# Kernel tuning notes

Measured on AMD Instinct MI355X. Metric: run time of the kernel, lower is better.

The kernel has to match this reference:

```python
import jax, jax.numpy as jnp
import numpy as np

DIM = 128      # transformer_dim = bottleneck_ch
NHEADS = 4
NEXP = 16
EHID = 256
WS = 8         # window_size
EPS = 1e-5     # LayerNorm eps


def setup_inputs() -> dict:
    key = jax.random.key(0)
    ks = jax.random.split(key, 6)
    B, H, W = 2, 128, 128
    N = H * W
    s = 0.02
    return {
        "x": jax.random.normal(ks[0], (B, N, DIM), jnp.float32),
        "ln1_g": jnp.ones((DIM,), jnp.float32),
        "ln1_b": jnp.zeros((DIM,), jnp.float32),
        "w_qkv": jax.random.normal(ks[1], (3 * DIM, DIM), jnp.float32) * s,
        "b_qkv": jnp.zeros((3 * DIM,), jnp.float32),
        "w_proj": jax.random.normal(ks[2], (DIM, DIM), jnp.float32) * s,
        "b_proj": jnp.zeros((DIM,), jnp.float32),
        "ln2_g": jnp.ones((DIM,), jnp.float32),
        "ln2_b": jnp.zeros((DIM,), jnp.float32),
        "gate_w": jax.random.normal(ks[3], (NEXP, DIM), jnp.float32) * s,
        "w1": jax.random.normal(ks[4], (NEXP, EHID, DIM), jnp.float32) * s,
        "b1": jnp.zeros((NEXP, EHID), jnp.float32),
        "w2": jax.random.normal(ks[5], (NEXP, DIM, EHID), jnp.float32) * s,
        "b2": jnp.zeros((NEXP, DIM), jnp.float32),
        "H": H,
        "W": W,
    }


def _ln(x, g, b):
    m = jnp.mean(x, axis=-1, keepdims=True)
    v = jnp.var(x, axis=-1, keepdims=True)
    return (x - m) * jax.lax.rsqrt(v + EPS) * g + b


def _win_attn(x, H, W, w_qkv, b_qkv, w_proj, b_proj):
    # x: (B, N, C); H,W divisible by WS (no padding branch needed)
    B, N, C = x.shape
    hd = C // NHEADS
    nH, nW = H // WS, W // WS
    # window partition: (B, N, C) -> (B*nH*nW, WS*WS, C)
    xw = x.reshape(B, nH, WS, nW, WS, C).transpose(0, 1, 3, 2, 4, 5)
    xw = xw.reshape(B * nH * nW, WS * WS, C)
    qkv = xw @ w_qkv.T + b_qkv
    q, k, v = jnp.split(qkv, 3, axis=-1)
    def heads(t):
        return t.reshape(-1, WS * WS, NHEADS, hd).transpose(0, 2, 1, 3)
    q, k, v = heads(q), heads(k), heads(v)
    scores = jnp.einsum('whqd,whkd->whqk', q, k) / jnp.sqrt(jnp.float32(hd))
    a = jax.nn.softmax(scores, axis=-1)
    o = jnp.einsum('whqk,whkd->whqd', a, v).transpose(0, 2, 1, 3)
    o = o.reshape(-1, WS * WS, C) @ w_proj.T + b_proj
    # window merge back to (B, N, C)
    o = o.reshape(B, nH, nW, WS, WS, C).transpose(0, 1, 3, 2, 4, 5)
    return o.reshape(B, N, C)


def _moe(x, gate_w, w1, b1, w2, b2):
    # top_k = 1 routing, eval mode (no noise / aux losses)
    B, N, C = x.shape
    f = x.reshape(-1, C)                      # (T, C)
    logits = f @ gate_w.T                     # (T, E)
    probs = jax.nn.softmax(logits, axis=-1)
    p = jnp.max(probs, axis=-1)               # top-1 prob
    idx = jnp.argmax(probs, axis=-1)          # top-1 expert id
    wgt = p / (p + 1e-8)                      # top_k_probs / (sum + eps)
    out = jnp.zeros_like(f)
    for e in range(NEXP):                     # small fixed expert loop
        h = jax.nn.gelu(f @ w1[e].T + b1[e], approximate=False)
        eo = h @ w2[e].T + b2[e]
        out = out + jnp.where((idx == e)[:, None], eo, 0.0)
    return (out * wgt[:, None]).reshape(B, N, C)


def reference(x, ln1_g, ln1_b, w_qkv, b_qkv, w_proj, b_proj,
              ln2_g, ln2_b, gate_w, w1, b1, w2, b2, H, W):
    x = x + _win_attn(_ln(x, ln1_g, ln1_b), H, W, w_qkv, b_qkv, w_proj, b_proj)
    x = x + _moe(_ln(x, ln2_g, ln2_b), gate_w, w1, b1, w2, b2)
    return x
```

## Files before the change

kernel.cpp:

```cpp
#include <hip/hip_runtime.h>
#include <math.h>

#define T_TOK 32768
#define DIM 128
#define NHEADS 4
#define HD 32
#define NEXP 16
#define EHID 256
#define NWIN 512
#define EPS 1e-5f
#define CPAD 16

typedef _Float16 f16x8 __attribute__((ext_vector_type(8)));
typedef _Float16 f16x4 __attribute__((ext_vector_type(4)));
typedef float f32x4v __attribute__((ext_vector_type(4)));

#define MFMA16(a, b, c) __builtin_amdgcn_mfma_f32_16x16x32_f16(a, b, c, 0, 0, 0)
#define LO_SCALE 4096.0f
#define LO_INV (1.0f / 4096.0f)

__device__ __forceinline__ int sw128(int r, int c) {
    return r * 128 + (((c >> 3) ^ (r & 7)) << 3) + (c & 7);
}
__device__ __forceinline__ int sw64(int r, int c) {
    return r * 64 + (((c >> 3) ^ (r & 7)) << 3) + (c & 7);
}
__device__ __forceinline__ int swht(int tok, int hid) {
    return tok * 256 + (((hid >> 3) ^ (tok & 7)) << 3) + (hid & 7);
}

__global__ __launch_bounds__(256) void k_cvt(
    const float* __restrict__ wqkv, const float* __restrict__ wproj,
    const float* __restrict__ w1, const float* __restrict__ w2,
    _Float16* __restrict__ wq_h, _Float16* __restrict__ wq_l,
    _Float16* __restrict__ wp_h, _Float16* __restrict__ wp_l,
    _Float16* __restrict__ w1h, _Float16* __restrict__ w2h,
    int* __restrict__ counts)
{
    int i = blockIdx.x * 256 + threadIdx.x;
    if (blockIdx.x == 0 && threadIdx.x < NEXP * CPAD) counts[threadIdx.x] = 0;
    {
        float4 a = ((const float4*)w1)[i];
        f16x4 h;
        h[0] = (_Float16)a.x; h[1] = (_Float16)a.y; h[2] = (_Float16)a.z; h[3] = (_Float16)a.w;
        *(f16x4*)(w1h + (size_t)i * 4) = h;
        float4 b = ((const float4*)w2)[i];
        f16x4 h2;
        h2[0] = (_Float16)b.x; h2[1] = (_Float16)b.y; h2[2] = (_Float16)b.z; h2[3] = (_Float16)b.w;
        *(f16x4*)(w2h + (size_t)i * 4) = h2;
    }
    if (i < 3 * DIM * DIM / 4) {
        float4 f = ((const float4*)wqkv)[i];
        float fv[4] = {f.x, f.y, f.z, f.w};
        f16x4 h, l;
        #pragma unroll
        for (int j = 0; j < 4; ++j) {
            _Float16 hh = (_Float16)fv[j];
            h[j] = hh;
            l[j] = (_Float16)((fv[j] - (float)hh) * LO_SCALE);
        }
        *(f16x4*)(wq_h + (size_t)i * 4) = h;
        *(f16x4*)(wq_l + (size_t)i * 4) = l;
    }
    if (i < DIM * DIM / 4) {
        float4 f = ((const float4*)wproj)[i];
        float fv[4] = {f.x, f.y, f.z, f.w};
        f16x4 h, l;
        #pragma unroll
        for (int j = 0; j < 4; ++j) {
            _Float16 hh = (_Float16)fv[j];
            h[j] = hh;
            l[j] = (_Float16)((fv[j] - (float)hh) * LO_SCALE);
        }
        *(f16x4*)(wp_h + (size_t)i * 4) = h;
        *(f16x4*)(wp_l + (size_t)i * 4) = l;
    }
}

__global__ __launch_bounds__(512) void k_attn(
    const float* __restrict__ x,
    const float* __restrict__ ln_g, const float* __restrict__ ln_b,
    const _Float16* __restrict__ wq_h, const _Float16* __restrict__ wq_l,
    const float* __restrict__ b_qkv,
    const _Float16* __restrict__ wp_h, const _Float16* __restrict__ wp_l,
    const float* __restrict__ b_proj,
    const float* __restrict__ ln2_g, const float* __restrict__ ln2_b,
    const float* __restrict__ gw,
    float* __restrict__ x2, _Float16* __restrict__ y2,
    float* __restrict__ wgt, int* __restrict__ perm, int* __restrict__ counts)
{
    __shared__ __align__(16) char smem[131072];
    _Float16* xoh = (_Float16*)(smem);
    _Float16* xol = (_Float16*)(smem + 16384);
    _Float16* qh  = (_Float16*)(smem + 32768);
    _Float16* ql  = (_Float16*)(smem + 49152);
    _Float16* kh  = (_Float16*)(smem + 65536);
    _Float16* kl  = (_Float16*)(smem + 81920);
    _Float16* vth = (_Float16*)(smem + 98304);
    _Float16* vtl = (_Float16*)(smem + 114688);
    float* xf   = (float*)(smem + 32768);
    float* ylds = (float*)(smem + 65792);
    float* lgs  = (float*)(smem + 98816);

    int tid = threadIdx.x;
    int w = tid >> 6, lane = tid & 63;
    int l15 = lane & 15, lg = lane >> 4;
    int wid = blockIdx.x;
    int wb = wid >> 8, wrr = (wid >> 4) & 15, wcc = wid & 15;
    const int tokbase = wb * 16384 + wrr * 1024 + wcc * 8;
    const size_t base = (size_t)tokbase * DIM;

    f16x8 qbh[3][4], qbl[3][4];
    float qbias[3];
    #pragma unroll
    for (int ct = 0; ct < 3; ++ct) {
        int o = w * 48 + ct * 16 + l15;
        qbias[ct] = b_qkv[o];
        #pragma unroll
        for (int ks = 0; ks < 4; ++ks) {
            size_t wo = (size_t)o * DIM + ks * 32 + lg * 8;
            qbh[ct][ks] = *(const f16x8*)(wq_h + wo);
            qbl[ct][ks] = *(const f16x8*)(wq_l + wo);
        }
    }
    float xres[16];
    {
        int rt = w & 3, cb = (w >> 2) * 64;
        #pragma unroll
        for (int ct = 0; ct < 4; ++ct) {
            int c = cb + ct * 16 + l15;
            #pragma unroll
            for (int r = 0; r < 4; ++r) {
                int q = rt * 16 + lg * 4 + r;
                xres[ct * 4 + r] = x[base + (size_t)(q >> 3) * 16384 + (size_t)(q & 7) * DIM + c];
            }
        }
    }

    {
        int tt = tid >> 3, sub = tid & 7;
        const float* xr = x + base + (size_t)(tt >> 3) * 16384 + (size_t)(tt & 7) * DIM + sub * 16;
        float v[16];
        float s = 0.f, sq = 0.f;
        #pragma unroll
        for (int j = 0; j < 4; ++j) {
            float4 t4 = *(const float4*)(xr + j * 4);
            v[4 * j] = t4.x; v[4 * j + 1] = t4.y; v[4 * j + 2] = t4.z; v[4 * j + 3] = t4.w;
            s += (t4.x + t4.y) + (t4.z + t4.w);
            sq = fmaf(t4.x, t4.x, fmaf(t4.y, t4.y, fmaf(t4.z, t4.z, fmaf(t4.w, t4.w, sq))));
        }
        s += __shfl_xor(s, 1); sq += __shfl_xor(sq, 1);
        s += __shfl_xor(s, 2); sq += __shfl_xor(sq, 2);
        s += __shfl_xor(s, 4); sq += __shfl_xor(sq, 4);
        float m = s * (1.f / DIM);
        float var = sq * (1.f / DIM) - m * m;
        float rs = rsqrtf(var + EPS);
        _Float16 hh[16], ll[16];
        #pragma unroll
        for (int j = 0; j < 16; ++j) {
            int k = sub * 16 + j;
            float a = (v[j] - m) * rs * ln_g[k] + ln_b[k];
            _Float16 h = (_Float16)a;
            hh[j] = h;
            ll[j] = (_Float16)((a - (float)h) * LO_SCALE);
        }
        *(f16x8*)&xoh[sw128(tt, sub * 16)]     = *(const f16x8*)&hh[0];
        *(f16x8*)&xoh[sw128(tt, sub * 16 + 8)] = *(const f16x8*)&hh[8];
        *(f16x8*)&xol[sw128(tt, sub * 16)]     = *(const f16x8*)&ll[0];
        *(f16x8*)&xol[sw128(tt, sub * 16 + 8)] = *(const f16x8*)&ll[8];
    }
    __syncthreads();

    #pragma unroll
    for (int ct = 0; ct < 3; ++ct) {
        int o = w * 48 + ct * 16 + l15;
        f32x4v am[4], ac[4];
        #pragma unroll
        for (int rt = 0; rt < 4; ++rt) { am[rt] = 0.0f; ac[rt] = 0.0f; }
        #pragma unroll
        for (int rt = 0; rt < 4; ++rt) {
            #pragma unroll
            for (int ks = 0; ks < 4; ++ks) {
                f16x8 ah = *(const f16x8*)&xoh[sw128(rt * 16 + l15, ks * 32 + lg * 8)];
                f16x8 al = *(const f16x8*)&xol[sw128(rt * 16 + l15, ks * 32 + lg * 8)];
                am[rt] = MFMA16(ah, qbh[ct][ks], am[rt]);
                ac[rt] = MFMA16(ah, qbl[ct][ks], ac[rt]);
                ac[rt] = MFMA16(al, qbh[ct][ks], ac[rt]);
            }
        }
        float bias = qbias[ct];
        if (o < 256) {
            #pragma unroll
            for (int rt = 0; rt < 4; ++rt) {
                #pragma unroll
                for (int r = 0; r < 4; ++r) {
                    int row = rt * 16 + lg * 4 + r;
                    float val = am[rt][r] + ac[rt][r] * LO_INV + bias;
                    _Float16 h = (_Float16)val;
                    _Float16 lo = (_Float16)((val - (float)h) * LO_SCALE);
                    if (o < 128) { qh[sw128(row, o)] = h;       ql[sw128(row, o)] = lo; }
                    else         { kh[sw128(row, o - 128)] = h; kl[sw128(row, o - 128)] = lo; }
                }
            }
        } else {
            int d = o - 256;
            #pragma unroll
            for (int rt = 0; rt < 4; ++rt) {
                f16x4 vh4, vl4;
                #pragma unroll
                for (int r = 0; r < 4; ++r) {
                    float val = am[rt][r] + ac[rt][r] * LO_INV + bias;
                    _Float16 h = (_Float16)val;
                    vh4[r] = h;
                    vl4[r] = (_Float16)((val - (float)h) * LO_SCALE);
                }
                int tok0 = rt * 16 + lg * 4;
                *(f16x4*)&vth[sw64(d, tok0)] = vh4;
                *(f16x4*)&vtl[sw64(d, tok0)] = vl4;
            }
        }
    }
    __syncthreads();

    const float scale = 0.17677669529663687f;
    int h = w & 3;
    int qo = h * HD, rgb = (w >> 2) * 2;
    float preg[2][4][4];
    {
        f16x8 kbh[4], kbl[4];
        #pragma unroll
        for (int ct = 0; ct < 4; ++ct) {
            kbh[ct] = *(const f16x8*)&kh[sw128(ct * 16 + l15, qo + lg * 8)];
            kbl[ct] = *(const f16x8*)&kl[sw128(ct * 16 + l15, qo + lg * 8)];
        }
        #pragma unroll
        for (int t = 0; t < 2; ++t) {
            int rg = rgb + t;
            f16x8 qah = *(const f16x8*)&qh[sw128(rg * 16 + l15, qo + lg * 8)];
            f16x8 qal = *(const f16x8*)&ql[sw128(rg * 16 + l15, qo + lg * 8)];
            f32x4v sm[4], sc2[4];
            #pragma unroll
            for (int ct = 0; ct < 4; ++ct) {
                sm[ct] = 0.0f; sc2[ct] = 0.0f;
                sm[ct] = MFMA16(qah, kbh[ct], sm[ct]);
                sc2[ct] = MFMA16(qah, kbl[ct], sc2[ct]);
                sc2[ct] = MFMA16(qal, kbh[ct], sc2[ct]);
            }
            #pragma unroll
            for (int r = 0; r < 4; ++r) {
                float v0 = (sm[0][r] + sc2[0][r] * LO_INV) * scale;
                float v1 = (sm[1][r] + sc2[1][r] * LO_INV) * scale;
                float v2 = (sm[2][r] + sc2[2][r] * LO_INV) * scale;
                float v3 = (sm[3][r] + sc2[3][r] * LO_INV) * scale;
                float mx = fmaxf(fmaxf(v0, v1), fmaxf(v2, v3));
                mx = fmaxf(mx, __shfl_xor(mx, 1));
                mx = fmaxf(mx, __shfl_xor(mx, 2));
                mx = fmaxf(mx, __shfl_xor(mx, 4));
                mx = fmaxf(mx, __shfl_xor(mx, 8));
                float e0 = expf(v0 - mx), e1 = expf(v1 - mx), e2 = expf(v2 - mx), e3 = expf(v3 - mx);
                float ss = (e0 + e1) + (e2 + e3);
                ss += __shfl_xor(ss, 1); ss += __shfl_xor(ss, 2);
                ss += __shfl_xor(ss, 4); ss += __shfl_xor(ss, 8);
                float inv = 1.f / ss;
                preg[t][0][r] = e0 * inv;
                preg[t][1][r] = e1 * inv;
                preg[t][2][r] = e2 * inv;
                preg[t][3][r] = e3 * inv;
            }
        }
    }
    __syncthreads();

    {
        _Float16* dsth = (h < 2) ? qh : kh;
        _Float16* dstl = (h < 2) ? ql : kl;
        int pb = (h & 1) * 4096;
        #pragma unroll
        for (int t = 0; t < 2; ++t) {
            int rg = rgb + t;
            #pragma unroll
            for (int ct = 0; ct < 4; ++ct) {
                #pragma unroll
                for (int r = 0; r < 4; ++r) {
                    float p = preg[t][ct][r];
                    int row = rg * 16 + lg * 4 + r, col = ct * 16 + l15;
                    _Float16 hh = (_Float16)p;
                    dsth[pb + sw64(row, col)] = hh;
                    dstl[pb + sw64(row, col)] = (_Float16)((p - (float)hh) * LO_SCALE);
                }
            }
        }
    }

    {
        const _Float16* psh = (h < 2) ? qh : kh;
        const _Float16* psl = (h < 2) ? ql : kl;
        int pb = (h & 1) * 4096;
        f16x8 vbh[2][2], vbl[2][2];
        #pragma unroll
        for (int ks = 0; ks < 2; ++ks)
            #pragma unroll
            for (int ct = 0; ct < 2; ++ct) {
                vbh[ks][ct] = *(const f16x8*)&vth[sw64(qo + ct * 16 + l15, ks * 32 + lg * 8)];
                vbl[ks][ct] = *(const f16x8*)&vtl[sw64(qo + ct * 16 + l15, ks * 32 + lg * 8)];
            }
        #pragma unroll
        for (int t = 0; t < 2; ++t) {
            int rg = rgb + t;
            f32x4v om[2], oc[2];
            om[0] = 0.0f; om[1] = 0.0f; oc[0] = 0.0f; oc[1] = 0.0f;
            #pragma unroll
            for (int ks = 0; ks < 2; ++ks) {
                f16x8 pah = *(const f16x8*)&psh[pb + sw64(rg * 16 + l15, ks * 32 + lg * 8)];
                f16x8 pal = *(const f16x8*)&psl[pb + sw64(rg * 16 + l15, ks * 32 + lg * 8)];
                #pragma unroll
                for (int ct = 0; ct < 2; ++ct) {
                    om[ct] = MFMA16(pah, vbh[ks][ct], om[ct]);
                    oc[ct] = MFMA16(pah, vbl[ks][ct], oc[ct]);
                    oc[ct] = MFMA16(pal, vbh[ks][ct], oc[ct]);
                }
            }
            #pragma unroll
            for (int ct = 0; ct < 2; ++ct) {
                #pragma unroll
                for (int r = 0; r < 4; ++r) {
                    float val = om[ct][r] + oc[ct][r] * LO_INV;
                    int row = rg * 16 + lg * 4 + r, col = qo + ct * 16 + l15;
                    _Float16 hh = (_Float16)val;
                    xoh[sw128(row, col)] = hh;
                    xol[sw128(row, col)] = (_Float16)((val - (float)hh) * LO_SCALE);
                }
            }
        }
    }

    f16x8 wpbh[4][4], wpbl[4][4];
    float pbias[4];
    {
        int cb = (w >> 2) * 64;
        #pragma unroll
        for (int ct = 0; ct < 4; ++ct) {
            int c = cb + ct * 16 + l15;
            pbias[ct] = b_proj[c];
            #pragma unroll
            for (int ks = 0; ks < 4; ++ks) {
                wpbh[ct][ks] = *(const f16x8*)(wp_h + (size_t)c * DIM + ks * 32 + lg * 8);
                wpbl[ct][ks] = *(const f16x8*)(wp_l + (size_t)c * DIM + ks * 32 + lg * 8);
            }
        }
    }
    __syncthreads();

    {
        int rt = w & 3, cb = (w >> 2) * 64;
        f32x4v pm[4], pc[4];
        #pragma unroll
        for (int ct = 0; ct < 4; ++ct) { pm[ct] = 0.0f; pc[ct] = 0.0f; }
        #pragma unroll
        for (int ks = 0; ks < 4; ++ks) {
            f16x8 ah = *(const f16x8*)&xoh[sw128(rt * 16 + l15, ks * 32 + lg * 8)];
            f16x8 al = *(const f16x8*)&xol[sw128(rt * 16 + l15, ks * 32 + lg * 8)];
            #pragma unroll
            for (int ct = 0; ct < 4; ++ct) {
                pm[ct] = MFMA16(ah, wpbh[ct][ks], pm[ct]);
                pc[ct] = MFMA16(ah, wpbl[ct][ks], pc[ct]);
                pc[ct] = MFMA16(al, wpbh[ct][ks], pc[ct]);
            }
        }
        #pragma unroll
        for (int ct = 0; ct < 4; ++ct) {
            int c = cb + ct * 16 + l15;
            #pragma unroll
            for (int r = 0; r < 4; ++r) {
                int q = rt * 16 + lg * 4 + r;
                xf[q * 129 + c] = xres[ct * 4 + r] + (pm[ct][r] + pc[ct][r] * LO_INV + pbias[ct]);
            }
        }
    }
    __syncthreads();

    float vrow[16];
    _Float16 yh[16];
    {
        int tt = tid >> 3, sub = tid & 7;
        const float* xr = xf + tt * 129 + sub * 16;
        float s = 0.f, sq = 0.f;
        #pragma unroll
        for (int j = 0; j < 16; ++j) {
            float t = xr[j];
            vrow[j] = t;
            s += t;
            sq = fmaf(t, t, sq);
        }
        s += __shfl_xor(s, 1); sq += __shfl_xor(sq, 1);
        s += __shfl_xor(s, 2); sq += __shfl_xor(sq, 2);
        s += __shfl_xor(s, 4); sq += __shfl_xor(sq, 4);
        float m = s * (1.f / DIM);
        float var = sq * (1.f / DIM) - m * m;
        float rs = rsqrtf(var + EPS);
        #pragma unroll
        for (int j = 0; j < 16; ++j) {
            int k = sub * 16 + j;
            float a = (vrow[j] - m) * rs * ln2_g[k] + ln2_b[k];
            ylds[tt * 129 + k] = a;
            yh[j] = (_Float16)a;
        }
    }
    __syncthreads();

    {
        int tk = tid & 63, eg = tid >> 6;
        const float* g0 = gw + (eg * 2 + 0) * DIM;
        const float* g1 = gw + (eg * 2 + 1) * DIM;
        float a0 = 0.f, a1 = 0.f;
        #pragma unroll 8
        for (int k = 0; k < DIM; ++k) {
            float yv = ylds[tk * 129 + k];
            a0 = fmaf(yv, g0[k], a0);
            a1 = fmaf(yv, g1[k], a1);
        }
        lgs[tk * 20 + eg * 2]     = a0;
        lgs[tk * 20 + eg * 2 + 1] = a1;
    }
    __syncthreads();

    if (tid < 64) {
        float mx = -1e30f; int am = 0;
        #pragma unroll
        for (int e = 0; e < NEXP; ++e) {
            float v = lgs[tid * 20 + e];
            if (v > mx) { mx = v; am = e; }
        }
        float ss = 0.f;
        #pragma unroll
        for (int e = 0; e < NEXP; ++e) ss += expf(lgs[tid * 20 + e] - mx);
        float p = 1.f / ss;
        int gtok = tokbase + (tid >> 3) * 128 + (tid & 7);
        wgt[gtok] = p / (p + 1e-8f);

        int myrank = 0, mycnt = 0;
        #pragma unroll
        for (int e = 0; e < NEXP; ++e) {
            unsigned long long mask = __ballot(am == e);
            if (am == e) myrank = (int)__popcll(mask & ((1ull << tid) - 1));
            if (tid == e) mycnt = (int)__popcll(mask);
        }
        int bky = 0;
        if (tid < NEXP) bky = atomicAdd(&counts[tid * CPAD], mycnt);
        bky = __shfl(bky, am);
        perm[(size_t)am * T_TOK + bky + myrank] = gtok;
    }

    {
        int tt = tid >> 3, sub = tid & 7;
        int gtok = tokbase + (tt >> 3) * 128 + (tt & 7);
        float4* dst = (float4*)(x2 + (size_t)gtok * DIM + sub * 16);
        #pragma unroll
        for (int j = 0; j < 4; ++j)
            dst[j] = make_float4(vrow[4 * j], vrow[4 * j + 1], vrow[4 * j + 2], vrow[4 * j + 3]);
        *(f16x8*)(y2 + (size_t)gtok * DIM + sub * 16)     = *(const f16x8*)&yh[0];
        *(f16x8*)(y2 + (size_t)gtok * DIM + sub * 16 + 8) = *(const f16x8*)&yh[8];
    }
}

__global__ __launch_bounds__(256, 3) void k_expert(
    const _Float16* __restrict__ y2, const float* __restrict__ x2,
    const _Float16* __restrict__ w1h, const float* __restrict__ b1,
    const _Float16* __restrict__ w2h, const float* __restrict__ b2,
    const int* __restrict__ perm, const int* __restrict__ counts,
    const float* __restrict__ wgt, float* __restrict__ out)
{
    __shared__ _Float16 yt[64 * 128];
    __shared__ _Float16 ht[64 * 256];
    __shared__ int rows[64];

    int bflat = blockIdx.x;
    int e = -1, tile = 0, acc0 = 0;
    #pragma unroll
    for (int ee = 0; ee < NEXP; ++ee) {
        int t = (counts[ee * CPAD] + 63) >> 6;
        if (e < 0 && bflat < acc0 + t) { e = ee; tile = bflat - acc0; }
        acc0 += t;
    }
    if (e < 0) return;
    int cnt = counts[e * CPAD];
    int row0 = tile << 6;
    int nr = min(64, cnt - row0);
    int tid = threadIdx.x, wv = tid >> 6, lane = tid & 63;
    int l15 = lane & 15, lg = lane >> 4;

    if (tid < 64) rows[tid] = (tid < nr) ? perm[(size_t)e * T_TOK + row0 + tid] : 0;
    __syncthreads();
    f16x8 vz = (_Float16)0.0f;
    for (int i = tid; i < 1024; i += 256) {
        int tt = i >> 4, k = (i & 15) * 8;
        f16x8 val = vz;
        if (tt < nr) val = *(const f16x8*)(y2 + (size_t)rows[tt] * DIM + k);
        *(f16x8*)&yt[sw128(tt, k)] = val;
    }
    __syncthreads();

    {
        f16x8 yb[4][4];
        #pragma unroll
        for (int ct = 0; ct < 4; ++ct)
            #pragma unroll
            for (int ks = 0; ks < 4; ++ks)
                yb[ct][ks] = *(const f16x8*)&yt[sw128(ct * 16 + l15, ks * 32 + lg * 8)];
        #pragma unroll
        for (int rt = 0; rt < 4; ++rt) {
            int hid_row = wv * 64 + rt * 16 + l15;
            f16x8 a1[4];
            #pragma unroll
            for (int ks = 0; ks < 4; ++ks)
                a1[ks] = *(const f16x8*)(w1h + ((size_t)e * EHID + hid_row) * DIM + ks * 32 + lg * 8);
            f32x4v acc[4];
            #pragma unroll
            for (int ct = 0; ct < 4; ++ct) acc[ct] = 0.0f;
            #pragma unroll
            for (int ct = 0; ct < 4; ++ct)
                #pragma unroll
                for (int ks = 0; ks < 4; ++ks)
                    acc[ct] = MFMA16(a1[ks], yb[ct][ks], acc[ct]);
            int hid0 = wv * 64 + rt * 16 + lg * 4;
            float4 bb4 = *(const float4*)(b1 + e * EHID + hid0);
            float bbv[4] = {bb4.x, bb4.y, bb4.z, bb4.w};
            #pragma unroll
            for (int ct = 0; ct < 4; ++ct) {
                f16x4 hv;
                #pragma unroll
                for (int r = 0; r < 4; ++r) {
                    float a = acc[ct][r] + bbv[r];
                    float gl = 0.5f * a * (1.f + erff(a * 0.70710678118654752f));
                    hv[r] = (_Float16)gl;
                }
                int tok = ct * 16 + l15;
                *(f16x4*)&ht[swht(tok, hid0)] = hv;
            }
        }
    }
    __syncthreads();

    {
        f16x8 wb[2][8];
        #pragma unroll
        for (int ct = 0; ct < 2; ++ct) {
            int c = wv * 32 + ct * 16 + l15;
            #pragma unroll
            for (int ks = 0; ks < 8; ++ks)
                wb[ct][ks] = *(const f16x8*)(w2h + ((size_t)e * DIM + c) * EHID + ks * 32 + lg * 8);
        }
        #pragma unroll
        for (int rt = 0; rt < 4; ++rt) {
            f16x8 af[8];
            #pragma unroll
            for (int ks = 0; ks < 8; ++ks)
                af[ks] = *(const f16x8*)&ht[swht(rt * 16 + l15, ks * 32 + lg * 8)];
            f32x4v acc2[2];
            acc2[0] = 0.0f; acc2[1] = 0.0f;
            #pragma unroll
            for (int ks = 0; ks < 8; ++ks)
                #pragma unroll
                for (int ct = 0; ct < 2; ++ct)
                    acc2[ct] = MFMA16(af[ks], wb[ct][ks], acc2[ct]);
            #pragma unroll
            for (int ct = 0; ct < 2; ++ct) {
                int c = wv * 32 + ct * 16 + l15;
                float bb = b2[e * DIM + c];
                #pragma unroll
                for (int r = 0; r < 4; ++r) {
                    int tt = rt * 16 + lg * 4 + r;
                    if (tt < nr) {
                        int gtok = rows[tt];
                        size_t go = (size_t)gtok * DIM + c;
                        out[go] = x2[go] + wgt[gtok] * (acc2[ct][r] + bb);
                    }
                }
            }
        }
    }
}

extern "C" void kernel_launch(void* const* d_in, const int* in_sizes, int n_in,
                              void* d_out, int out_size, void* d_ws, size_t ws_size,
                              hipStream_t stream) {
    const float* x      = (const float*)d_in[0];
    const float* ln1_g  = (const float*)d_in[1];
    const float* ln1_b  = (const float*)d_in[2];
    const float* w_qkv  = (const float*)d_in[3];
    const float* b_qkv  = (const float*)d_in[4];
    const float* w_proj = (const float*)d_in[5];
    const float* b_proj = (const float*)d_in[6];
    const float* ln2_g  = (const float*)d_in[7];
    const float* ln2_b  = (const float*)d_in[8];
    const float* gate_w = (const float*)d_in[9];
    const float* w1     = (const float*)d_in[10];
    const float* b1     = (const float*)d_in[11];
    const float* w2     = (const float*)d_in[12];
    const float* b2     = (const float*)d_in[13];
    float* out = (float*)d_out;

    char* p = (char*)d_ws;
    float* x2 = (float*)p;                 p += (size_t)T_TOK * DIM * 4;
    _Float16* y2 = (_Float16*)p;           p += (size_t)T_TOK * DIM * 2;
    _Float16* wq_h = (_Float16*)p;         p += 3 * DIM * DIM * 2;
    _Float16* wq_l = (_Float16*)p;         p += 3 * DIM * DIM * 2;
    _Float16* wp_h = (_Float16*)p;         p += DIM * DIM * 2;
    _Float16* wp_l = (_Float16*)p;         p += DIM * DIM * 2;
    _Float16* w1h = (_Float16*)p;          p += NEXP * EHID * DIM * 2;
    _Float16* w2h = (_Float16*)p;          p += NEXP * EHID * DIM * 2;
    float* wgt = (float*)p;                p += T_TOK * 4;
    int* perm = (int*)p;                   p += (size_t)NEXP * T_TOK * 4;
    int* counts = (int*)p;                 p += NEXP * CPAD * 4;

    k_cvt<<<512, 256, 0, stream>>>(w_qkv, w_proj, w1, w2, wq_h, wq_l, wp_h, wp_l,
                                   w1h, w2h, counts);
    k_attn<<<NWIN, 512, 0, stream>>>(x, ln1_g, ln1_b, wq_h, wq_l, b_qkv,
                                     wp_h, wp_l, b_proj, ln2_g, ln2_b, gate_w,
                                     x2, y2, wgt, perm, counts);
    k_expert<<<544, 256, 0, stream>>>(y2, x2, w1h, b1, w2h, b2, perm, counts, wgt, out);
}
```

Baseline: 114.1 us.

## Double attention block to 1024 threads, splitting per-wave work in half

The window-attention kernel now runs 16 waves per block instead of 8. QKV projection, score/softmax, PV, output projection, LayerNorm and gate-logit work are each split across the extra waves, so every wave handles half as many tiles. The goal is more latency hiding and fewer registers per thread for a grid of only 512 blocks, at the cost of more barrier participants and an uneven QKV split (waves 8-15 do one tile, waves 0-7 do two).

```diff
diff --git a/kernel.cpp b/kernel.cpp
--- a/kernel.cpp
+++ b/kernel.cpp
@@ -77,7 +77,7 @@
     }
 }
 
-__global__ __launch_bounds__(512) void k_attn(
+__global__ __launch_bounds__(1024) void k_attn(
     const float* __restrict__ x,
     const float* __restrict__ ln_g, const float* __restrict__ ln_b,
     const _Float16* __restrict__ wq_h, const _Float16* __restrict__ wq_l,
@@ -110,24 +110,25 @@
     const int tokbase = wb * 16384 + wrr * 1024 + wcc * 8;
     const size_t base = (size_t)tokbase * DIM;
 
-    f16x8 qbh[3][4], qbl[3][4];
-    float qbias[3];
+    f16x8 qbh[2][4], qbl[2][4];
+    float qbias[2];
     #pragma unroll
-    for (int ct = 0; ct < 3; ++ct) {
-        int o = w * 48 + ct * 16 + l15;
-        qbias[ct] = b_qkv[o];
+    for (int tl = 0; tl < 2; ++tl) {
+        if (tl == 1 && w >= 8) break;
+        int o = ((tl == 0) ? w : 16 + w) * 16 + l15;
+        qbias[tl] = b_qkv[o];
         #pragma unroll
         for (int ks = 0; ks < 4; ++ks) {
             size_t wo = (size_t)o * DIM + ks * 32 + lg * 8;
-            qbh[ct][ks] = *(const f16x8*)(wq_h + wo);
-            qbl[ct][ks] = *(const f16x8*)(wq_l + wo);
-        }
-    }
-    float xres[16];
-    {
-        int rt = w & 3, cb = (w >> 2) * 64;
-        #pragma unroll
-        for (int ct = 0; ct < 4; ++ct) {
+            qbh[tl][ks] = *(const f16x8*)(wq_h + wo);
+            qbl[tl][ks] = *(const f16x8*)(wq_l + wo);
+        }
+    }
+    float xres[8];
+    {
+        int rt = w & 3, cb = (w >> 2) * 32;
+        #pragma unroll
+        for (int ct = 0; ct < 2; ++ct) {
             int c = cb + ct * 16 + l15;
             #pragma unroll
             for (int r = 0; r < 4; ++r) {
@@ -138,12 +139,12 @@
     }
 
     {
-        int tt = tid >> 3, sub = tid & 7;
-        const float* xr = x + base + (size_t)(tt >> 3) * 16384 + (size_t)(tt & 7) * DIM + sub * 16;
-        float v[16];
+        int tt = tid >> 4, sub = tid & 15;
+        const float* xr = x + base + (size_t)(tt >> 3) * 16384 + (size_t)(tt & 7) * DIM + sub * 8;
+        float v[8];
         float s = 0.f, sq = 0.f;
         #pragma unroll
-        for (int j = 0; j < 4; ++j) {
+        for (int j = 0; j < 2; ++j) {
             float4 t4 = *(const float4*)(xr + j * 4);
             v[4 * j] = t4.x; v[4 * j + 1] = t4.y; v[4 * j + 2] = t4.z; v[4 * j + 3] = t4.w;
             s += (t4.x + t4.y) + (t4.z + t4.w);
@@ -152,28 +153,28 @@
         s += __shfl_xor(s, 1); sq += __shfl_xor(sq, 1);
         s += __shfl_xor(s, 2); sq += __shfl_xor(sq, 2);
         s += __shfl_xor(s, 4); sq += __shfl_xor(sq, 4);
+        s += __shfl_xor(s, 8); sq += __shfl_xor(sq, 8);
         float m = s * (1.f / DIM);
         float var = sq * (1.f / DIM) - m * m;
         float rs = rsqrtf(var + EPS);
-        _Float16 hh[16], ll[16];
-        #pragma unroll
-        for (int j = 0; j < 16; ++j) {
-            int k = sub * 16 + j;
+        _Float16 hh[8], ll[8];
+        #pragma unroll
+        for (int j = 0; j < 8; ++j) {
+            int k = sub * 8 + j;
             float a = (v[j] - m) * rs * ln_g[k] + ln_b[k];
             _Float16 h = (_Float16)a;
             hh[j] = h;
             ll[j] = (_Float16)((a - (float)h) * LO_SCALE);
         }
-        *(f16x8*)&xoh[sw128(tt, sub * 16)]     = *(const f16x8*)&hh[0];
-        *(f16x8*)&xoh[sw128(tt, sub * 16 + 8)] = *(const f16x8*)&hh[8];
-        *(f16x8*)&xol[sw128(tt, sub * 16)]     = *(const f16x8*)&ll[0];
-        *(f16x8*)&xol[sw128(tt, sub * 16 + 8)] = *(const f16x8*)&ll[8];
+        *(f16x8*)&xoh[sw128(tt, sub * 8)] = *(const f16x8*)&hh[0];
+        *(f16x8*)&xol[sw128(tt, sub * 8)] = *(const f16x8*)&ll[0];
     }
     __syncthreads();
 
     #pragma unroll
-    for (int ct = 0; ct < 3; ++ct) {
-        int o = w * 48 + ct * 16 + l15;
+    for (int tl = 0; tl < 2; ++tl) {
+        if (tl == 1 && w >= 8) break;
+        int o = ((tl == 0) ? w : 16 + w) * 16 + l15;
         f32x4v am[4], ac[4];
         #pragma unroll
         for (int rt = 0; rt < 4; ++rt) { am[rt] = 0.0f; ac[rt] = 0.0f; }
@@ -183,12 +184,12 @@
             for (int ks = 0; ks < 4; ++ks) {
                 f16x8 ah = *(const f16x8*)&xoh[sw128(rt * 16 + l15, ks * 32 + lg * 8)];
                 f16x8 al = *(const f16x8*)&xol[sw128(rt * 16 + l15, ks * 32 + lg * 8)];
-                am[rt] = MFMA16(ah, qbh[ct][ks], am[rt]);
-                ac[rt] = MFMA16(ah, qbl[ct][ks], ac[rt]);
-                ac[rt] = MFMA16(al, qbh[ct][ks], ac[rt]);
-            }
-        }
-        float bias = qbias[ct];
+                am[rt] = MFMA16(ah, qbh[tl][ks], am[rt]);
+                ac[rt] = MFMA16(ah, qbl[tl][ks], ac[rt]);
+                ac[rt] = MFMA16(al, qbh[tl][ks], ac[rt]);
+            }
+        }
+        float bias = qbias[tl];
         if (o < 256) {
             #pragma unroll
             for (int rt = 0; rt < 4; ++rt) {
@@ -224,8 +225,8 @@
 
     const float scale = 0.17677669529663687f;
     int h = w & 3;
-    int qo = h * HD, rgb = (w >> 2) * 2;
-    float preg[2][4][4];
+    int qo = h * HD, rg = w >> 2;
+    float preg[4][4];
     {
         f16x8 kbh[4], kbl[4];
         #pragma unroll
@@ -233,40 +234,36 @@
             kbh[ct] = *(const f16x8*)&kh[sw128(ct * 16 + l15, qo + lg * 8)];
             kbl[ct] = *(const f16x8*)&kl[sw128(ct * 16 + l15, qo + lg * 8)];
         }
-        #pragma unroll
-        for (int t = 0; t < 2; ++t) {
-            int rg = rgb + t;
-            f16x8 qah = *(const f16x8*)&qh[sw128(rg * 16 + l15, qo + lg * 8)];
-            f16x8 qal = *(const f16x8*)&ql[sw128(rg * 16 + l15, qo + lg * 8)];
-            f32x4v sm[4], sc2[4];
-            #pragma unroll
-            for (int ct = 0; ct < 4; ++ct) {
-                sm[ct] = 0.0f; sc2[ct] = 0.0f;
-                sm[ct] = MFMA16(qah, kbh[ct], sm[ct]);
-                sc2[ct] = MFMA16(qah, kbl[ct], sc2[ct]);
-                sc2[ct] = MFMA16(qal, kbh[ct], sc2[ct]);
-            }
-            #pragma unroll
-            for (int r = 0; r < 4; ++r) {
-                float v0 = (sm[0][r] + sc2[0][r] * LO_INV) * scale;
-                float v1 = (sm[1][r] + sc2[1][r] * LO_INV) * scale;
-                float v2 = (sm[2][r] + sc2[2][r] * LO_INV) * scale;
-                float v3 = (sm[3][r] + sc2[3][r] * LO_INV) * scale;
-                float mx = fmaxf(fmaxf(v0, v1), fmaxf(v2, v3));
-                mx = fmaxf(mx, __shfl_xor(mx, 1));
-                mx = fmaxf(mx, __shfl_xor(mx, 2));
-                mx = fmaxf(mx, __shfl_xor(mx, 4));
-                mx = fmaxf(mx, __shfl_xor(mx, 8));
-                float e0 = expf(v0 - mx), e1 = expf(v1 - mx), e2 = expf(v2 - mx), e3 = expf(v3 - mx);
-                float ss = (e0 + e1) + (e2 + e3);
-                ss += __shfl_xor(ss, 1); ss += __shfl_xor(ss, 2);
-                ss += __shfl_xor(ss, 4); ss += __shfl_xor(ss, 8);
-                float inv = 1.f / ss;
-                preg[t][0][r] = e0 * inv;
-                preg[t][1][r] = e1 * inv;
-                preg[t][2][r] = e2 * inv;
-                preg[t][3][r] = e3 * inv;
-            }
+        f16x8 qah = *(const f16x8*)&qh[sw128(rg * 16 + l15, qo + lg * 8)];
+        f16x8 qal = *(const f16x8*)&ql[sw128(rg * 16 + l15, qo + lg * 8)];
+        f32x4v sm[4], sc2[4];
+        #pragma unroll
+        for (int ct = 0; ct < 4; ++ct) {
+            sm[ct] = 0.0f; sc2[ct] = 0.0f;
+            sm[ct] = MFMA16(qah, kbh[ct], sm[ct]);
+            sc2[ct] = MFMA16(qah, kbl[ct], sc2[ct]);
+            sc2[ct] = MFMA16(qal, kbh[ct], sc2[ct]);
+        }
+        #pragma unroll
+        for (int r = 0; r < 4; ++r) {
+            float v0 = (sm[0][r] + sc2[0][r] * LO_INV) * scale;
+            float v1 = (sm[1][r] + sc2[1][r] * LO_INV) * scale;
+            float v2 = (sm[2][r] + sc2[2][r] * LO_INV) * scale;
+            float v3 = (sm[3][r] + sc2[3][r] * LO_INV) * scale;
+            float mx = fmaxf(fmaxf(v0, v1), fmaxf(v2, v3));
+            mx = fmaxf(mx, __shfl_xor(mx, 1));
+            mx = fmaxf(mx, __shfl_xor(mx, 2));
+            mx = fmaxf(mx, __shfl_xor(mx, 4));
+            mx = fmaxf(mx, __shfl_xor(mx, 8));
+            float e0 = expf(v0 - mx), e1 = expf(v1 - mx), e2 = expf(v2 - mx), e3 = expf(v3 - mx);
+            float ss = (e0 + e1) + (e2 + e3);
+            ss += __shfl_xor(ss, 1); ss += __shfl_xor(ss, 2);
+            ss += __shfl_xor(ss, 4); ss += __shfl_xor(ss, 8);
+            float inv = 1.f / ss;
+            preg[0][r] = e0 * inv;
+            preg[1][r] = e1 * inv;
+            preg[2][r] = e2 * inv;
+            preg[3][r] = e3 * inv;
         }
     }
     __syncthreads();
@@ -276,18 +273,14 @@
         _Float16* dstl = (h < 2) ? ql : kl;
         int pb = (h & 1) * 4096;
         #pragma unroll
-        for (int t = 0; t < 2; ++t) {
-            int rg = rgb + t;
-            #pragma unroll
-            for (int ct = 0; ct < 4; ++ct) {
-                #pragma unroll
-                for (int r = 0; r < 4; ++r) {
-                    float p = preg[t][ct][r];
-                    int row = rg * 16 + lg * 4 + r, col = ct * 16 + l15;
-                    _Float16 hh = (_Float16)p;
-                    dsth[pb + sw64(row, col)] = hh;
-                    dstl[pb + sw64(row, col)] = (_Float16)((p - (float)hh) * LO_SCALE);
-                }
+        for (int ct = 0; ct < 4; ++ct) {
+            #pragma unroll
+            for (int r = 0; r < 4; ++r) {
+                float p = preg[ct][r];
+                int row = rg * 16 + lg * 4 + r, col = ct * 16 + l15;
+                _Float16 hh = (_Float16)p;
+                dsth[pb + sw64(row, col)] = hh;
+                dstl[pb + sw64(row, col)] = (_Float16)((p - (float)hh) * LO_SCALE);
             }
         }
     }
@@ -304,42 +297,38 @@
                 vbh[ks][ct] = *(const f16x8*)&vth[sw64(qo + ct * 16 + l15, ks * 32 + lg * 8)];
                 vbl[ks][ct] = *(const f16x8*)&vtl[sw64(qo + ct * 16 + l15, ks * 32 + lg * 8)];
             }
-        #pragma unroll
-        for (int t = 0; t < 2; ++t) {
-            int rg = rgb + t;
-            f32x4v om[2], oc[2];
-            om[0] = 0.0f; om[1] = 0.0f; oc[0] = 0.0f; oc[1] = 0.0f;
-            #pragma unroll
-            for (int ks = 0; ks < 2; ++ks) {
-                f16x8 pah = *(const f16x8*)&psh[pb + sw64(rg * 16 + l15, ks * 32 + lg * 8)];
-                f16x8 pal = *(const f16x8*)&psl[pb + sw64(rg * 16 + l15, ks * 32 + lg * 8)];
-                #pragma unroll
-                for (int ct = 0; ct < 2; ++ct) {
-                    om[ct] = MFMA16(pah, vbh[ks][ct], om[ct]);
-                    oc[ct] = MFMA16(pah, vbl[ks][ct], oc[ct]);
-                    oc[ct] = MFMA16(pal, vbh[ks][ct], oc[ct]);
-                }
-            }
+        f32x4v om[2], oc[2];
+        om[0] = 0.0f; om[1] = 0.0f; oc[0] = 0.0f; oc[1] = 0.0f;
+        #pragma unroll
+        for (int ks = 0; ks < 2; ++ks) {
+            f16x8 pah = *(const f16x8*)&psh[pb + sw64(rg * 16 + l15, ks * 32 + lg * 8)];
+            f16x8 pal = *(const f16x8*)&psl[pb + sw64(rg * 16 + l15, ks * 32 + lg * 8)];
             #pragma unroll
             for (int ct = 0; ct < 2; ++ct) {
-                #pragma unroll
-                for (int r = 0; r < 4; ++r) {
-                    float val = om[ct][r] + oc[ct][r] * LO_INV;
-                    int row = rg * 16 + lg * 4 + r, col = qo + ct * 16 + l15;
-                    _Float16 hh = (_Float16)val;
-                    xoh[sw128(row, col)] = hh;
-                    xol[sw128(row, col)] = (_Float16)((val - (float)hh) * LO_SCALE);
-                }
-            }
-        }
-    }
-
-    f16x8 wpbh[4][4], wpbl[4][4];
-    float pbias[4];
-    {
-        int cb = (w >> 2) * 64;
-        #pragma unroll
-        for (int ct = 0; ct < 4; ++ct) {
+                om[ct] = MFMA16(pah, vbh[ks][ct], om[ct]);
+                oc[ct] = MFMA16(pah, vbl[ks][ct], oc[ct]);
+                oc[ct] = MFMA16(pal, vbh[ks][ct], oc[ct]);
+            }
+        }
+        #pragma unroll
+        for (int ct = 0; ct < 2; ++ct) {
+            #pragma unroll
+            for (int r = 0; r < 4; ++r) {
+                float val = om[ct][r] + oc[ct][r] * LO_INV;
+                int row = rg * 16 + lg * 4 + r, col = qo + ct * 16 + l15;
+                _Float16 hh = (_Float16)val;
+                xoh[sw128(row, col)] = hh;
+                xol[sw128(row, col)] = (_Float16)((val - (float)hh) * LO_SCALE);
+            }
+        }
+    }
+
+    f16x8 wpbh[2][4], wpbl[2][4];
+    float pbias[2];
+    {
+        int cb = (w >> 2) * 32;
+        #pragma unroll
+        for (int ct = 0; ct < 2; ++ct) {
             int c = cb + ct * 16 + l15;
             pbias[ct] = b_proj[c];
             #pragma unroll
@@ -352,23 +341,22 @@
     __syncthreads();
 
     {
-        int rt = w & 3, cb = (w >> 2) * 64;
-        f32x4v pm[4], pc[4];
-        #pragma unroll
-        for (int ct = 0; ct < 4; ++ct) { pm[ct] = 0.0f; pc[ct] = 0.0f; }
+        int rt = w & 3, cb = (w >> 2) * 32;
+        f32x4v pm[2], pc[2];
+        pm[0] = 0.0f; pm[1] = 0.0f; pc[0] = 0.0f; pc[1] = 0.0f;
         #pragma unroll
         for (int ks = 0; ks < 4; ++ks) {
             f16x8 ah = *(const f16x8*)&xoh[sw128(rt * 16 + l15, ks * 32 + lg * 8)];
             f16x8 al = *(const f16x8*)&xol[sw128(rt * 16 + l15, ks * 32 + lg * 8)];
             #pragma unroll
-            for (int ct = 0; ct < 4; ++ct) {
+            for (int ct = 0; ct < 2; ++ct) {
                 pm[ct] = MFMA16(ah, wpbh[ct][ks], pm[ct]);
                 pc[ct] = MFMA16(ah, wpbl[ct][ks], pc[ct]);
                 pc[ct] = MFMA16(al, wpbh[ct][ks], pc[ct]);
             }
         }
         #pragma unroll
-        for (int ct = 0; ct < 4; ++ct) {
+        for (int ct = 0; ct < 2; ++ct) {
             int c = cb + ct * 16 + l15;
             #pragma unroll
             for (int r = 0; r < 4; ++r) {
@@ -379,14 +367,14 @@
     }
     __syncthreads();
 
-    float vrow[16];
-    _Float16 yh[16];
-    {
-        int tt = tid >> 3, sub = tid & 7;
-        const float* xr = xf + tt * 129 + sub * 16;
+    float vrow[8];
+    _Float16 yh[8];
+    {
+        int tt = tid >> 4, sub = tid & 15;
+        const float* xr = xf + tt * 129 + sub * 8;
         float s = 0.f, sq = 0.f;
         #pragma unroll
-        for (int j = 0; j < 16; ++j) {
+        for (int j = 0; j < 8; ++j) {
             float t = xr[j];
             vrow[j] = t;
             s += t;
@@ -395,12 +383,13 @@
         s += __shfl_xor(s, 1); sq += __shfl_xor(sq, 1);
         s += __shfl_xor(s, 2); sq += __shfl_xor(sq, 2);
         s += __shfl_xor(s, 4); sq += __shfl_xor(sq, 4);
+        s += __shfl_xor(s, 8); sq += __shfl_xor(sq, 8);
         float m = s * (1.f / DIM);
         float var = sq * (1.f / DIM) - m * m;
         float rs = rsqrtf(var + EPS);
         #pragma unroll
-        for (int j = 0; j < 16; ++j) {
-            int k = sub * 16 + j;
+        for (int j = 0; j < 8; ++j) {
+            int k = sub * 8 + j;
             float a = (vrow[j] - m) * rs * ln2_g[k] + ln2_b[k];
             ylds[tt * 129 + k] = a;
             yh[j] = (_Float16)a;
@@ -410,17 +399,16 @@
 
     {
         int tk = tid & 63, eg = tid >> 6;
-        const float* g0 = gw + (eg * 2 + 0) * DIM;
-        const float* g1 = gw + (eg * 2 + 1) * DIM;
-        float a0 = 0.f, a1 = 0.f;
-        #pragma unroll 8
-        for (int k = 0; k < DIM; ++k) {
-            float yv = ylds[tk * 129 + k];
-            a0 = fmaf(yv, g0[k], a0);
-            a1 = fmaf(yv, g1[k], a1);
-        }
-        lgs[tk * 20 + eg * 2]     = a0;
-        lgs[tk * 20 + eg * 2 + 1] = a1;
+        const float* g0 = gw + eg * DIM;
+        float a0 = 0.f, a1 = 0.f, a2 = 0.f, a3 = 0.f;
+        #pragma unroll 4
+        for (int k = 0; k < DIM; k += 4) {
+            a0 = fmaf(ylds[tk * 129 + k],     g0[k],     a0);
+            a1 = fmaf(ylds[tk * 129 + k + 1], g0[k + 1], a1);
+            a2 = fmaf(ylds[tk * 129 + k + 2], g0[k + 2], a2);
+            a3 = fmaf(ylds[tk * 129 + k + 3], g0[k + 3], a3);
+        }
+        lgs[tk * 20 + eg] = (a0 + a1) + (a2 + a3);
     }
     __syncthreads();
 
@@ -452,14 +440,12 @@
     }
 
     {
-        int tt = tid >> 3, sub = tid & 7;
+        int tt = tid >> 4, sub = tid & 15;
         int gtok = tokbase + (tt >> 3) * 128 + (tt & 7);
-        float4* dst = (float4*)(x2 + (size_t)gtok * DIM + sub * 16);
-        #pragma unroll
-        for (int j = 0; j < 4; ++j)
-            dst[j] = make_float4(vrow[4 * j], vrow[4 * j + 1], vrow[4 * j + 2], vrow[4 * j + 3]);
-        *(f16x8*)(y2 + (size_t)gtok * DIM + sub * 16)     = *(const f16x8*)&yh[0];
-        *(f16x8*)(y2 + (size_t)gtok * DIM + sub * 16 + 8) = *(const f16x8*)&yh[8];
+        float4* dst = (float4*)(x2 + (size_t)gtok * DIM + sub * 8);
+        dst[0] = make_float4(vrow[0], vrow[1], vrow[2], vrow[3]);
+        dst[1] = make_float4(vrow[4], vrow[5], vrow[6], vrow[7]);
+        *(f16x8*)(y2 + (size_t)gtok * DIM + sub * 8) = *(const f16x8*)&yh[0];
     }
 }
 
@@ -615,8 +601,8 @@
 
     k_cvt<<<512, 256, 0, stream>>>(w_qkv, w_proj, w1, w2, wq_h, wq_l, wp_h, wp_l,
                                    w1h, w2h, counts);
-    k_attn<<<NWIN, 512, 0, stream>>>(x, ln1_g, ln1_b, wq_h, wq_l, b_qkv,
-                                     wp_h, wp_l, b_proj, ln2_g, ln2_b, gate_w,
-                                     x2, y2, wgt, perm, counts);
+    k_attn<<<NWIN, 1024, 0, stream>>>(x, ln1_g, ln1_b, wq_h, wq_l, b_qkv,
+                                      wp_h, wp_l, b_proj, ln2_g, ln2_b, gate_w,
+                                      x2, y2, wgt, perm, counts);
     k_expert<<<544, 256, 0, stream>>>(y2, x2, w1h, b1, w2h, b2, perm, counts, wgt, out);
 }
```

Result: faster. 105.3 us (-7.8%).
